# Performance work log

Hardware: AMD Instinct MI355X
Metric: run time of the kernel (lower is better)

## Reference

```python
import jax, jax.numpy as jnp
from jax import lax
import numpy as np

NPOINT = 1024   # S: number of sampled centroids
NSAMPLE = 32    # K: neighbors per centroid (unmasked ball query = k-nearest via argsort)


def _gather(p, i):
    # p: [B,N,C], i: [B,...] int -> [B,...,C]
    return jax.vmap(lambda pb, ib: pb[ib])(p, i)


def _fps(xyz, farthest_init, npoint):
    # Iterative farthest point sampling, faithful to the torch loop.
    B, N, _ = xyz.shape
    dist0 = jnp.full((B, N), 1e10, dtype=xyz.dtype)

    def step(carry, _):
        distance, farthest = carry
        centroid = jnp.take_along_axis(xyz, farthest[:, None, None], axis=1)  # [B,1,3]
        d = jnp.sum((xyz - centroid) ** 2, -1)          # [B,N]
        distance = jnp.minimum(distance, d)
        return (distance, jnp.argmax(distance, -1)), farthest

    _, cent = lax.scan(step, (dist0, farthest_init.astype(jnp.int32)), None, length=npoint)
    return cent.T  # [B, npoint]


def _sq_dist(src, dst):
    # src: [B,S,3], dst: [B,N,3] -> [B,S,N]
    return (jnp.sum(src ** 2, -1)[:, :, None]
            + jnp.sum(dst ** 2, -1)[:, None, :]
            - 2.0 * jnp.einsum('bsc,bnc->bsn', src, dst))


def setup_inputs() -> dict:
    key = jax.random.key(0)
    ks = jax.random.split(key, 6)
    B, N, C = 8, 4096, 6
    inp = {
        'xyz': jax.random.normal(ks[0], (B, N, 3), jnp.float32),
        'points': jax.random.normal(ks[1], (B, N, C), jnp.float32),
        'farthest_init': jax.random.randint(ks[2], (B,), 0, N),
    }
    dims = [C + 3, 64, 64, 128]
    for li in range(3):
        inp[f'w{li}'] = jax.random.normal(ks[3 + li], (dims[li + 1], dims[li]), jnp.float32) * 0.1
        inp[f'b{li}'] = jnp.zeros((dims[li + 1],), jnp.float32)
    return inp


def reference(xyz, points, farthest_init, w0, b0, w1, b1, w2, b2):
    fps_idx = _fps(xyz, farthest_init, NPOINT)            # [B,S]
    new_xyz = _gather(xyz, fps_idx)                       # [B,S,3]
    dist = _sq_dist(new_xyz, xyz)                         # [B,S,N]
    _, idx = lax.top_k(-dist, NSAMPLE)                    # k-nearest == argsort[:, :, :K]
    g_xyz = _gather(xyz, idx) - new_xyz[:, :, None, :]    # [B,S,K,3]
    g_pts = _gather(points, idx)                          # [B,S,K,C]
    h = jnp.concatenate([g_xyz, g_pts], axis=-1)          # [B,S,K,C+3]
    for w, b in ((w0, b0), (w1, b1), (w2, b2)):           # 1x1 conv MLP + relu
        h = jax.nn.relu(jnp.einsum('bskc,oc->bsko', h, w) + b)
    new_points = jnp.max(h, axis=2)                       # max-pool over K -> [B,S,128]
    return new_xyz, new_points
```

## Files before the change

kernel.cpp:

```cpp
#include <hip/hip_runtime.h>

#define INF_F 3.402823466e+38f
typedef unsigned long long u64;
typedef __attribute__((ext_vector_type(2))) float f32x2;

__device__ __forceinline__ float f_add(float a, float b){ return __fadd_rn(a,b); }
__device__ __forceinline__ float f_sub(float a, float b){ return __fsub_rn(a,b); }
__device__ __forceinline__ float f_mul(float a, float b){ return __fmul_rn(a,b); }

__device__ __forceinline__ f32x2 pk_add(f32x2 a, f32x2 b){ f32x2 d; asm("v_pk_add_f32 %0, %1, %2" : "=v"(d) : "v"(a), "v"(b)); return d; }
__device__ __forceinline__ f32x2 pk_mul(f32x2 a, f32x2 b){ f32x2 d; asm("v_pk_mul_f32 %0, %1, %2" : "=v"(d) : "v"(a), "v"(b)); return d; }

template<int CTRL>
__device__ __forceinline__ double dpp_d(double x) {
    u64 u = (u64)__double_as_longlong(x);
    int lo = __builtin_amdgcn_update_dpp(0, (int)(unsigned)u,        CTRL, 0xF, 0xF, true);
    int hi = __builtin_amdgcn_update_dpp(0, (int)(unsigned)(u>>32), CTRL, 0xF, 0xF, true);
    return __longlong_as_double((long long)(((u64)(unsigned)hi << 32) | (unsigned)lo));
}
template<int CTRL>
__device__ __forceinline__ float dpp_f(float x) {
    int r = __builtin_amdgcn_update_dpp(0, __float_as_int(x), CTRL, 0xF, 0xF, true);
    return __int_as_float(r);
}
__device__ __forceinline__ double swz16_d(double x) {
    u64 u = (u64)__double_as_longlong(x);
    int lo = __builtin_amdgcn_ds_swizzle((int)(unsigned)u,        0x401F);
    int hi = __builtin_amdgcn_ds_swizzle((int)(unsigned)(u>>32), 0x401F);
    return __longlong_as_double((long long)(((u64)(unsigned)hi << 32) | (unsigned)lo));
}
__device__ __forceinline__ float swz16_f(float x) {
    return __int_as_float(__builtin_amdgcn_ds_swizzle(__float_as_int(x), 0x401F));
}
__device__ __forceinline__ double readlane_d(double x, int l) {
    u64 u = (u64)__double_as_longlong(x);
    int lo = __builtin_amdgcn_readlane((int)(unsigned)u,        l);
    int hi = __builtin_amdgcn_readlane((int)(unsigned)(u>>32), l);
    return __longlong_as_double((long long)(((u64)(unsigned)hi << 32) | (unsigned)lo));
}
__device__ __forceinline__ double pack_key(float nd, unsigned low) {
    return __longlong_as_double((long long)(((u64)__float_as_uint(nd) << 32) | (u64)low));
}

__global__ __launch_bounds__(256, 1) void fps_kernel(
    const float* __restrict__ xyz, const int* __restrict__ farthest_init,
    float* __restrict__ out_new_xyz)
{
    const int b    = blockIdx.x;
    const int tid  = threadIdx.x;
    const int lane = tid & 63;
    const int wid  = tid >> 6;

    __shared__ float  sx[4096], sy[4096], sz[4096];
    __shared__ int    hist[1024];
    __shared__ double red[2][4];

    const float* xb = xyz + (size_t)b * 4096 * 3;
    for (int n = tid; n < 4096; n += 256) {
        sx[n] = xb[n*3+0]; sy[n] = xb[n*3+1]; sz[n] = xb[n*3+2];
    }
    __syncthreads();

    f32x2 px[8], py[8], pz[8], dist2[8];
    #pragma unroll
    for (int jp = 0; jp < 8; ++jp) {
        const int n0 = (2*jp) * 256 + tid, n1 = n0 + 256;
        px[jp] = (f32x2){sx[n0], sx[n1]};
        py[jp] = (f32x2){sy[n0], sy[n1]};
        pz[jp] = (f32x2){sz[n0], sz[n1]};
        dist2[jp] = (f32x2){1e10f, 1e10f};
    }
    const unsigned lowbase = 4095u - (unsigned)tid;

    int far = farthest_init[b];
    int p = 0;
    #pragma unroll 1
    for (int it = 0; it < 1024; ++it) {
        if (tid == 0) hist[it] = far;
        const float cx = sx[far], cy = sy[far], cz = sz[far];
        const f32x2 ncx = (f32x2){-cx, -cx};
        const f32x2 ncy = (f32x2){-cy, -cy};
        const f32x2 ncz = (f32x2){-cz, -cz};

        double a0 = -1.0, a1 = -1.0, a2 = -1.0, a3 = -1.0;
        #pragma unroll
        for (int jp = 0; jp < 8; ++jp) {
            f32x2 dx = pk_add(px[jp], ncx);
            f32x2 dy = pk_add(py[jp], ncy);
            f32x2 dz = pk_add(pz[jp], ncz);
            f32x2 d2 = pk_add(pk_add(pk_mul(dx,dx), pk_mul(dy,dy)), pk_mul(dz,dz));
            float nd0 = fminf(dist2[jp][0], d2[0]); dist2[jp][0] = nd0;
            float nd1 = fminf(dist2[jp][1], d2[1]); dist2[jp][1] = nd1;
            double k0 = pack_key(nd0, lowbase - (unsigned)((2*jp)*256));
            double k1 = pack_key(nd1, lowbase - (unsigned)((2*jp+1)*256));
            if (jp & 1) { a2 = fmax(a2, k0); a3 = fmax(a3, k1); }
            else        { a0 = fmax(a0, k0); a1 = fmax(a1, k1); }
        }
        double best = fmax(fmax(a0, a1), fmax(a2, a3));
        best = fmax(best, dpp_d<0xB1>(best));
        best = fmax(best, dpp_d<0x4E>(best));
        best = fmax(best, dpp_d<0x141>(best));
        best = fmax(best, dpp_d<0x140>(best));
        best = fmax(best, swz16_d(best));
        double wb = fmax(readlane_d(best, 0), readlane_d(best, 32));
        if (lane == 0) red[p][wid] = wb;
        __syncthreads();
        double g = fmax(fmax(red[p][0], red[p][1]), fmax(red[p][2], red[p][3]));
        far = 4095 - (int)(unsigned)((u64)__double_as_longlong(g) & 0xFFFFFFFFull);
        p ^= 1;
    }
    __syncthreads();
    #pragma unroll
    for (int q = 0; q < 4; ++q) {
        int s  = q * 256 + tid;
        int id = hist[s];
        float* o = out_new_xyz + ((size_t)b * 1024 + s) * 3;
        o[0] = sx[id]; o[1] = sy[id]; o[2] = sz[id];
    }
}

template<int G>
__device__ __forceinline__ double rebuild8(const double (&key)[64], double w) {
    const double DINF = __builtin_huge_val();
    double m = DINF;
    #pragma unroll
    for (int e = 0; e < 8; ++e) {
        double v = key[G*8+e];
        v = (v > w) ? v : DINF;
        m = fmin(m, v);
    }
    return m;
}

__global__ __launch_bounds__(256, 1) void knn_kernel(
    const float* __restrict__ xyz, const float* __restrict__ new_xyz,
    int* __restrict__ out_idx)
{
    const int tid  = threadIdx.x;
    const int lane = tid & 63;
    const int wid  = tid >> 6;
    const int blk  = blockIdx.x * 4 + wid;
    const int b    = blk >> 10;
    const double DINF = __builtin_huge_val();

    const float* xb = xyz + (size_t)b * 4096 * 3;
    const float* cp = new_xyz + (size_t)blk * 3;
    const float cx = cp[0], cy = cp[1], cz = cp[2];
    const float src2 = f_add(f_add(f_mul(cx,cx), f_mul(cy,cy)), f_mul(cz,cz));

    double key[64];
    #pragma unroll
    for (int j = 0; j < 64; ++j) {
        const int n = j * 64 + lane;
        const float* pt = xb + n * 3;
        float x = pt[0], y = pt[1], z = pt[2];
        float dst2 = f_add(f_add(f_mul(x,x), f_mul(y,y)), f_mul(z,z));
        float dot  = f_add(f_add(f_mul(cx,x), f_mul(cy,y)), f_mul(cz,z));
        float d = f_sub(f_add(src2, dst2), f_mul(2.0f, dot));
        key[j] = __longlong_as_double((long long)(((u64)__float_as_uint(d) << 32) | (u64)(unsigned)n));
    }

    double gm[8];
    #pragma unroll
    for (int g = 0; g < 8; ++g) {
        double m = key[g*8];
        #pragma unroll
        for (int e = 1; e < 8; ++e) m = fmin(m, key[g*8+e]);
        gm[g] = m;
    }

    double w = -1.0;
    int myidx = 0;
    #pragma unroll 1
    for (int t = 0; t < 32; ++t) {
        double lm = fmin(fmin(fmin(gm[0], gm[1]), fmin(gm[2], gm[3])),
                         fmin(fmin(gm[4], gm[5]), fmin(gm[6], gm[7])));
        lm = fmin(lm, dpp_d<0xB1>(lm));
        lm = fmin(lm, dpp_d<0x4E>(lm));
        lm = fmin(lm, dpp_d<0x141>(lm));
        lm = fmin(lm, dpp_d<0x140>(lm));
        lm = fmin(lm, swz16_d(lm));
        double gmin = fmin(readlane_d(lm, 0), readlane_d(lm, 32));
        int n = (int)(unsigned)((u64)__double_as_longlong(gmin) & 0xFFFFFFFFull);
        if (lane == t) myidx = n;
        w = gmin;
        const int gs = __builtin_amdgcn_readfirstlane(n >> 9);
        switch (gs) {
            case 0: gm[0] = rebuild8<0>(key, w); break;
            case 1: gm[1] = rebuild8<1>(key, w); break;
            case 2: gm[2] = rebuild8<2>(key, w); break;
            case 3: gm[3] = rebuild8<3>(key, w); break;
            case 4: gm[4] = rebuild8<4>(key, w); break;
            case 5: gm[5] = rebuild8<5>(key, w); break;
            case 6: gm[6] = rebuild8<6>(key, w); break;
            case 7: gm[7] = rebuild8<7>(key, w); break;
        }
    }
    if (lane < 32) out_idx[(size_t)blk * 32 + lane] = myidx;
}

__global__ __launch_bounds__(256, 1) void mlp_kernel(
    const float* __restrict__ xyz, const float* __restrict__ points,
    const int* __restrict__ knn_idx,
    const float* __restrict__ w0, const float* __restrict__ b0,
    const float* __restrict__ w1, const float* __restrict__ b1,
    const float* __restrict__ w2, const float* __restrict__ b2,
    const float* __restrict__ new_xyz, float* __restrict__ out_np)
{
    const int tid = threadIdx.x;
    const int k   = tid & 31;
    const int gs  = blockIdx.x * 8 + (tid >> 5);
    const int b   = gs >> 10;
    const int n   = knn_idx[(size_t)gs * 32 + k];

    const float cx = new_xyz[gs*3+0], cy = new_xyz[gs*3+1], cz = new_xyz[gs*3+2];
    const float* pxyz = xyz + ((size_t)b * 4096 + n) * 3;
    float h0[9];
    h0[0] = pxyz[0] - cx;
    h0[1] = pxyz[1] - cy;
    h0[2] = pxyz[2] - cz;
    const float* pp = points + ((size_t)b * 4096 + n) * 6;
    #pragma unroll
    for (int c = 0; c < 6; ++c) h0[3 + c] = pp[c];

    float h1[64];
    #pragma unroll
    for (int o = 0; o < 64; ++o) {
        float acc = b0[o];
        #pragma unroll
        for (int c = 0; c < 9; ++c) acc = fmaf(h0[c], w0[o*9+c], acc);
        h1[o] = fmaxf(acc, 0.0f);
    }

    float h2[64];
    #pragma unroll
    for (int o = 0; o < 64; ++o) {
        float acc = b1[o];
        #pragma unroll
        for (int c = 0; c < 64; ++c) acc = fmaf(h1[c], w1[o*64+c], acc);
        h2[o] = fmaxf(acc, 0.0f);
    }

    float* outp = out_np + (size_t)gs * 128;
    for (int og = 0; og < 4; ++og) {
        float keep = 0.0f;
        for (int o2 = 0; o2 < 32; ++o2) {
            const int o = og * 32 + o2;
            float acc = b2[o];
            #pragma unroll
            for (int c = 0; c < 64; ++c) acc = fmaf(h2[c], w2[o*64+c], acc);
            float m = fmaxf(acc, 0.0f);
            m = fmaxf(m, dpp_f<0xB1>(m));
            m = fmaxf(m, dpp_f<0x4E>(m));
            m = fmaxf(m, dpp_f<0x141>(m));
            m = fmaxf(m, dpp_f<0x140>(m));
            m = fmaxf(m, swz16_f(m));
            keep = (k == o2) ? m : keep;
        }
        outp[og * 32 + k] = keep;
    }
}

__global__ __launch_bounds__(256) void knn_mlp_kernel(
    const float* __restrict__ xyz, const float* __restrict__ points,
    const float* __restrict__ w0, const float* __restrict__ b0,
    const float* __restrict__ w1, const float* __restrict__ b1,
    const float* __restrict__ w2, const float* __restrict__ b2,
    const float* __restrict__ new_xyz, float* __restrict__ out_np)
{
    const int blk    = blockIdx.x;
    const int b      = blk >> 7;
    const int s_base = (blk & 127) * 8;
    const int tid    = threadIdx.x;
    const int lane   = tid & 63;
    const int wid    = tid >> 6;

    __shared__ float sx[4096], sy[4096], sz[4096];
    __shared__ float cent[8][3];
    __shared__ int   idxbuf[8][32];

    const float* xb = xyz + (size_t)b * 4096 * 3;
    for (int n = tid; n < 4096; n += 256) {
        sx[n] = xb[n*3+0]; sy[n] = xb[n*3+1]; sz[n] = xb[n*3+2];
    }
    if (tid < 24) ((float*)cent)[tid] = new_xyz[((size_t)b * 1024 + s_base) * 3 + tid];
    __syncthreads();

    for (int si = 0; si < 2; ++si) {
        const int sl = wid * 2 + si;
        const float cx = cent[sl][0], cy = cent[sl][1], cz = cent[sl][2];
        const float src2 = f_add(f_add(f_mul(cx,cx), f_mul(cy,cy)), f_mul(cz,cz));
        float d[64];
        #pragma unroll
        for (int j = 0; j < 64; ++j) {
            int n = j * 64 + lane;
            float x = sx[n], y = sy[n], z = sz[n];
            float dst2 = f_add(f_add(f_mul(x,x), f_mul(y,y)), f_mul(z,z));
            float dot  = f_add(f_add(f_mul(cx,x), f_mul(cy,y)), f_mul(cz,z));
            d[j] = f_sub(f_add(src2, dst2), f_mul(2.0f, dot));
        }
        int myg  = 0;
        int prev = -1;
        for (int t = 0; t < 32; ++t) {
            float bv = INF_F; int bi = 0x7fffffff;
            #pragma unroll
            for (int j = 0; j < 64; ++j) {
                int n = j * 64 + lane;
                if (n == prev) d[j] = INF_F;
                float v = d[j];
                if (v < bv) { bv = v; bi = n; }
            }
            #pragma unroll
            for (int m = 1; m < 64; m <<= 1) {
                float ov = __shfl_xor(bv, m);
                int   oi = __shfl_xor(bi, m);
                if (ov < bv || (ov == bv && oi < bi)) { bv = ov; bi = oi; }
            }
            if (lane == t) myg = bi;
            prev = bi;
        }
        if (lane < 32) idxbuf[sl][lane] = myg;
    }
    __syncthreads();

    const int k   = tid & 31;
    const int sl2 = tid >> 5;
    const int s   = s_base + sl2;
    const int n   = idxbuf[sl2][k];

    const float cx = cent[sl2][0], cy = cent[sl2][1], cz = cent[sl2][2];
    float h0[9];
    h0[0] = sx[n] - cx;
    h0[1] = sy[n] - cy;
    h0[2] = sz[n] - cz;
    const float* pp = points + ((size_t)b * 4096 + n) * 6;
    #pragma unroll
    for (int c = 0; c < 6; ++c) h0[3 + c] = pp[c];

    float h1[64];
    #pragma unroll
    for (int o = 0; o < 64; ++o) {
        float acc = b0[o];
        #pragma unroll
        for (int c = 0; c < 9; ++c) acc = fmaf(h0[c], w0[o*9+c], acc);
        h1[o] = fmaxf(acc, 0.0f);
    }
    float h2[64];
    #pragma unroll
    for (int o = 0; o < 64; ++o) {
        float acc = b1[o];
        #pragma unroll
        for (int c = 0; c < 64; ++c) acc = fmaf(h1[c], w1[o*64+c], acc);
        h2[o] = fmaxf(acc, 0.0f);
    }
    float* outp = out_np + ((size_t)b * 1024 + s) * 128;
    for (int og = 0; og < 4; ++og) {
        float keep = 0.0f;
        for (int o2 = 0; o2 < 32; ++o2) {
            const int o = og * 32 + o2;
            float acc = b2[o];
            #pragma unroll
            for (int c = 0; c < 64; ++c) acc = fmaf(h2[c], w2[o*64+c], acc);
            float m = fmaxf(acc, 0.0f);
            #pragma unroll
            for (int mm = 1; mm < 32; mm <<= 1)
                m = fmaxf(m, __shfl_xor(m, mm));
            keep = (k == o2) ? m : keep;
        }
        outp[og * 32 + k] = keep;
    }
}

extern "C" void kernel_launch(void* const* d_in, const int* in_sizes, int n_in,
                              void* d_out, int out_size, void* d_ws, size_t ws_size,
                              hipStream_t stream) {
    const float* xyz           = (const float*)d_in[0];
    const float* points        = (const float*)d_in[1];
    const int*   farthest_init = (const int*)  d_in[2];
    const float* w0 = (const float*)d_in[3];
    const float* b0 = (const float*)d_in[4];
    const float* w1 = (const float*)d_in[5];
    const float* b1 = (const float*)d_in[6];
    const float* w2 = (const float*)d_in[7];
    const float* b2 = (const float*)d_in[8];

    float* out        = (float*)d_out;
    float* new_xyz    = out;
    float* new_points = out + 8 * 1024 * 3;

    fps_kernel<<<8, 256, 0, stream>>>(xyz, farthest_init, new_xyz);

    if (ws_size >= (size_t)(8192 * 32 * sizeof(int))) {
        int* knn_idx = (int*)d_ws;
        knn_kernel<<<2048, 256, 0, stream>>>(xyz, new_xyz, knn_idx);
        mlp_kernel<<<1024, 256, 0, stream>>>(xyz, points, knn_idx,
                                             w0, b0, w1, b1, w2, b2,
                                             new_xyz, new_points);
    } else {
        knn_mlp_kernel<<<1024, 256, 0, stream>>>(xyz, points, w0, b0, w1, b1, w2, b2,
                                                 new_xyz, new_points);
    }
}
```

Before: 772.4 us.

## Use DPP row-broadcast reductions, carry centroid coords through FPS reduction, pack MLP FMAs

Wave-wide max/min reductions now use DPP row_bcast steps with a final readlane instead of ds_swizzle plus two readlanes. In FPS, each wave reads the winning point's coordinates from registers and publishes them with its key, so the next iteration skips the dependent LDS lookup of the centroid. The MLP kernel's 64-wide layers now use packed v_pk_fma_f32 with split accumulators, which changes the summation order slightly. The goal is a shorter serial critical path per FPS iteration and fewer instructions in the MLP, at the cost of a large switch on the selected register.

```diff
diff --git a/kernel.cpp b/kernel.cpp
--- a/kernel.cpp
+++ b/kernel.cpp
@@ -10,24 +10,19 @@
 
 __device__ __forceinline__ f32x2 pk_add(f32x2 a, f32x2 b){ f32x2 d; asm("v_pk_add_f32 %0, %1, %2" : "=v"(d) : "v"(a), "v"(b)); return d; }
 __device__ __forceinline__ f32x2 pk_mul(f32x2 a, f32x2 b){ f32x2 d; asm("v_pk_mul_f32 %0, %1, %2" : "=v"(d) : "v"(a), "v"(b)); return d; }
-
-template<int CTRL>
+__device__ __forceinline__ f32x2 pk_fma(f32x2 a, f32x2 b, f32x2 c){ f32x2 d; asm("v_pk_fma_f32 %0, %1, %2, %3" : "=v"(d) : "v"(a), "v"(b), "v"(c)); return d; }
+
+template<int CTRL, int RM, unsigned OLDLO, unsigned OLDHI>
 __device__ __forceinline__ double dpp_d(double x) {
     u64 u = (u64)__double_as_longlong(x);
-    int lo = __builtin_amdgcn_update_dpp(0, (int)(unsigned)u,        CTRL, 0xF, 0xF, true);
-    int hi = __builtin_amdgcn_update_dpp(0, (int)(unsigned)(u>>32), CTRL, 0xF, 0xF, true);
+    int lo = __builtin_amdgcn_update_dpp((int)OLDLO, (int)(unsigned)u,        CTRL, RM, 0xF, true);
+    int hi = __builtin_amdgcn_update_dpp((int)OLDHI, (int)(unsigned)(u>>32), CTRL, RM, 0xF, true);
     return __longlong_as_double((long long)(((u64)(unsigned)hi << 32) | (unsigned)lo));
 }
 template<int CTRL>
 __device__ __forceinline__ float dpp_f(float x) {
     int r = __builtin_amdgcn_update_dpp(0, __float_as_int(x), CTRL, 0xF, 0xF, true);
     return __int_as_float(r);
-}
-__device__ __forceinline__ double swz16_d(double x) {
-    u64 u = (u64)__double_as_longlong(x);
-    int lo = __builtin_amdgcn_ds_swizzle((int)(unsigned)u,        0x401F);
-    int hi = __builtin_amdgcn_ds_swizzle((int)(unsigned)(u>>32), 0x401F);
-    return __longlong_as_double((long long)(((u64)(unsigned)hi << 32) | (unsigned)lo));
 }
 __device__ __forceinline__ float swz16_f(float x) {
     return __int_as_float(__builtin_amdgcn_ds_swizzle(__float_as_int(x), 0x401F));
@@ -38,8 +33,30 @@
     int hi = __builtin_amdgcn_readlane((int)(unsigned)(u>>32), l);
     return __longlong_as_double((long long)(((u64)(unsigned)hi << 32) | (unsigned)lo));
 }
+__device__ __forceinline__ float readlane_f(float x, int l) {
+    return __int_as_float(__builtin_amdgcn_readlane(__float_as_int(x), l));
+}
 __device__ __forceinline__ double pack_key(float nd, unsigned low) {
     return __longlong_as_double((long long)(((u64)__float_as_uint(nd) << 32) | (u64)low));
+}
+
+__device__ __forceinline__ double wave_max_key(double k) {
+    k = fmax(k, dpp_d<0xB1, 0xF, 0u, 0u>(k));
+    k = fmax(k, dpp_d<0x4E, 0xF, 0u, 0u>(k));
+    k = fmax(k, dpp_d<0x141,0xF, 0u, 0u>(k));
+    k = fmax(k, dpp_d<0x140,0xF, 0u, 0u>(k));
+    k = fmax(k, dpp_d<0x142,0xE, 0u, 0u>(k));
+    k = fmax(k, dpp_d<0x143,0xC, 0u, 0u>(k));
+    return readlane_d(k, 63);
+}
+__device__ __forceinline__ double wave_min_key(double k) {
+    k = fmin(k, dpp_d<0xB1, 0xF, 0u, 0x7FF00000u>(k));
+    k = fmin(k, dpp_d<0x4E, 0xF, 0u, 0x7FF00000u>(k));
+    k = fmin(k, dpp_d<0x141,0xF, 0u, 0x7FF00000u>(k));
+    k = fmin(k, dpp_d<0x140,0xF, 0u, 0x7FF00000u>(k));
+    k = fmin(k, dpp_d<0x142,0xE, 0u, 0x7FF00000u>(k));
+    k = fmin(k, dpp_d<0x143,0xC, 0u, 0x7FF00000u>(k));
+    return readlane_d(k, 63);
 }
 
 __global__ __launch_bounds__(256, 1) void fps_kernel(
@@ -54,6 +71,7 @@
     __shared__ float  sx[4096], sy[4096], sz[4096];
     __shared__ int    hist[1024];
     __shared__ double red[2][4];
+    __shared__ float  redc[2][4][3];
 
     const float* xb = xyz + (size_t)b * 4096 * 3;
     for (int n = tid; n < 4096; n += 256) {
@@ -73,11 +91,11 @@
     const unsigned lowbase = 4095u - (unsigned)tid;
 
     int far = farthest_init[b];
+    float cx = sx[far], cy = sy[far], cz = sz[far];
     int p = 0;
     #pragma unroll 1
     for (int it = 0; it < 1024; ++it) {
         if (tid == 0) hist[it] = far;
-        const float cx = sx[far], cy = sy[far], cz = sz[far];
         const f32x2 ncx = (f32x2){-cx, -cx};
         const f32x2 ncy = (f32x2){-cy, -cy};
         const f32x2 ncz = (f32x2){-cz, -cz};
@@ -96,16 +114,49 @@
             if (jp & 1) { a2 = fmax(a2, k0); a3 = fmax(a3, k1); }
             else        { a0 = fmax(a0, k0); a1 = fmax(a1, k1); }
         }
-        double best = fmax(fmax(a0, a1), fmax(a2, a3));
-        best = fmax(best, dpp_d<0xB1>(best));
-        best = fmax(best, dpp_d<0x4E>(best));
-        best = fmax(best, dpp_d<0x141>(best));
-        best = fmax(best, dpp_d<0x140>(best));
-        best = fmax(best, swz16_d(best));
-        double wb = fmax(readlane_d(best, 0), readlane_d(best, 32));
-        if (lane == 0) red[p][wid] = wb;
+        double wkey = wave_max_key(fmax(fmax(a0, a1), fmax(a2, a3)));
+
+        const unsigned wlow = (unsigned)((u64)__double_as_longlong(wkey) & 0xFFFFFFFFull);
+        const int n_w   = 4095 - (int)wlow;
+        const int jsel  = n_w >> 8;
+        const int olane = n_w & 63;
+        float sxv, syv, szv;
+        switch (jsel) {
+            case  0: sxv=px[0][0]; syv=py[0][0]; szv=pz[0][0]; break;
+            case  1: sxv=px[0][1]; syv=py[0][1]; szv=pz[0][1]; break;
+            case  2: sxv=px[1][0]; syv=py[1][0]; szv=pz[1][0]; break;
+            case  3: sxv=px[1][1]; syv=py[1][1]; szv=pz[1][1]; break;
+            case  4: sxv=px[2][0]; syv=py[2][0]; szv=pz[2][0]; break;
+            case  5: sxv=px[2][1]; syv=py[2][1]; szv=pz[2][1]; break;
+            case  6: sxv=px[3][0]; syv=py[3][0]; szv=pz[3][0]; break;
+            case  7: sxv=px[3][1]; syv=py[3][1]; szv=pz[3][1]; break;
+            case  8: sxv=px[4][0]; syv=py[4][0]; szv=pz[4][0]; break;
+            case  9: sxv=px[4][1]; syv=py[4][1]; szv=pz[4][1]; break;
+            case 10: sxv=px[5][0]; syv=py[5][0]; szv=pz[5][0]; break;
+            case 11: sxv=px[5][1]; syv=py[5][1]; szv=pz[5][1]; break;
+            case 12: sxv=px[6][0]; syv=py[6][0]; szv=pz[6][0]; break;
+            case 13: sxv=px[6][1]; syv=py[6][1]; szv=pz[6][1]; break;
+            case 14: sxv=px[7][0]; syv=py[7][0]; szv=pz[7][0]; break;
+            default: sxv=px[7][1]; syv=py[7][1]; szv=pz[7][1]; break;
+        }
+        const float cwx = readlane_f(sxv, olane);
+        const float cwy = readlane_f(syv, olane);
+        const float cwz = readlane_f(szv, olane);
+        if (lane == 0) {
+            red[p][wid] = wkey;
+            redc[p][wid][0] = cwx; redc[p][wid][1] = cwy; redc[p][wid][2] = cwz;
+        }
         __syncthreads();
-        double g = fmax(fmax(red[p][0], red[p][1]), fmax(red[p][2], red[p][3]));
+        const double k0 = red[p][0], k1 = red[p][1], k2 = red[p][2], k3 = red[p][3];
+        const bool s1 = k1 > k0;
+        const bool s3 = k3 > k2;
+        const double k01 = s1 ? k1 : k0;
+        const double k23 = s3 ? k3 : k2;
+        const bool sf = k23 > k01;
+        const double g = sf ? k23 : k01;
+        const int i01 = s1 ? 1 : 0, i23 = s3 ? 3 : 2;
+        const int iw  = sf ? i23 : i01;
+        cx = redc[p][iw][0]; cy = redc[p][iw][1]; cz = redc[p][iw][2];
         far = 4095 - (int)(unsigned)((u64)__double_as_longlong(g) & 0xFFFFFFFFull);
         p ^= 1;
     }
@@ -141,7 +192,6 @@
     const int wid  = tid >> 6;
     const int blk  = blockIdx.x * 4 + wid;
     const int b    = blk >> 10;
-    const double DINF = __builtin_huge_val();
 
     const float* xb = xyz + (size_t)b * 4096 * 3;
     const float* cp = new_xyz + (size_t)blk * 3;
@@ -175,12 +225,7 @@
     for (int t = 0; t < 32; ++t) {
         double lm = fmin(fmin(fmin(gm[0], gm[1]), fmin(gm[2], gm[3])),
                          fmin(fmin(gm[4], gm[5]), fmin(gm[6], gm[7])));
-        lm = fmin(lm, dpp_d<0xB1>(lm));
-        lm = fmin(lm, dpp_d<0x4E>(lm));
-        lm = fmin(lm, dpp_d<0x141>(lm));
-        lm = fmin(lm, dpp_d<0x140>(lm));
-        lm = fmin(lm, swz16_d(lm));
-        double gmin = fmin(readlane_d(lm, 0), readlane_d(lm, 32));
+        double gmin = wave_min_key(lm);
         int n = (int)(unsigned)((u64)__double_as_longlong(gmin) & 0xFFFFFFFFull);
         if (lane == t) myidx = n;
         w = gmin;
@@ -223,33 +268,42 @@
     #pragma unroll
     for (int c = 0; c < 6; ++c) h0[3 + c] = pp[c];
 
-    float h1[64];
-    #pragma unroll
-    for (int o = 0; o < 64; ++o) {
-        float acc = b0[o];
-        #pragma unroll
-        for (int c = 0; c < 9; ++c) acc = fmaf(h0[c], w0[o*9+c], acc);
-        h1[o] = fmaxf(acc, 0.0f);
-    }
-
-    float h2[64];
-    #pragma unroll
-    for (int o = 0; o < 64; ++o) {
-        float acc = b1[o];
-        #pragma unroll
-        for (int c = 0; c < 64; ++c) acc = fmaf(h1[c], w1[o*64+c], acc);
-        h2[o] = fmaxf(acc, 0.0f);
-    }
-
+    f32x2 h1p[32];
+    #pragma unroll
+    for (int o = 0; o < 64; o += 2) {
+        float accA = b0[o], accB = b0[o+1];
+        #pragma unroll
+        for (int c = 0; c < 9; ++c) {
+            accA = fmaf(h0[c], w0[o*9+c],     accA);
+            accB = fmaf(h0[c], w0[(o+1)*9+c], accB);
+        }
+        h1p[o>>1] = (f32x2){fmaxf(accA, 0.0f), fmaxf(accB, 0.0f)};
+    }
+
+    const f32x2* w1v = (const f32x2*)w1;
+    f32x2 h2p[32];
+    #pragma unroll
+    for (int o = 0; o < 64; o += 2) {
+        f32x2 accA = (f32x2){b1[o],   0.0f};
+        f32x2 accB = (f32x2){b1[o+1], 0.0f};
+        #pragma unroll
+        for (int i = 0; i < 32; ++i) {
+            accA = pk_fma(h1p[i], w1v[o*32+i],     accA);
+            accB = pk_fma(h1p[i], w1v[(o+1)*32+i], accB);
+        }
+        h2p[o>>1] = (f32x2){fmaxf(accA[0]+accA[1], 0.0f), fmaxf(accB[0]+accB[1], 0.0f)};
+    }
+
+    const f32x2* w2v = (const f32x2*)w2;
     float* outp = out_np + (size_t)gs * 128;
     for (int og = 0; og < 4; ++og) {
         float keep = 0.0f;
         for (int o2 = 0; o2 < 32; ++o2) {
             const int o = og * 32 + o2;
-            float acc = b2[o];
+            f32x2 acc = (f32x2){b2[o], 0.0f};
             #pragma unroll
-            for (int c = 0; c < 64; ++c) acc = fmaf(h2[c], w2[o*64+c], acc);
-            float m = fmaxf(acc, 0.0f);
+            for (int i = 0; i < 32; ++i) acc = pk_fma(h2p[i], w2v[o*32+i], acc);
+            float m = fmaxf(acc[0] + acc[1], 0.0f);
             m = fmaxf(m, dpp_f<0xB1>(m));
             m = fmaxf(m, dpp_f<0x4E>(m));
             m = fmaxf(m, dpp_f<0x141>(m));
```

New measurement: 957.1 us. 23.9% more time.
